# Optimization experiments

Hardware: AMD Instinct MI355X
Metric: run time of the kernel (lower is better)

Reference implementation:

```python
import jax, jax.numpy as jnp
import numpy as np

B, D, M, P, I, O = 256, 10, 32, 36, 8, 16
NUM_ITERATIONS = 3
EPS = 1e-07


def squash(s, axis=-1):
    sq = jnp.sum(s * s, axis=axis, keepdims=True)
    safe_norm = jnp.sqrt(sq + EPS)
    scale = sq / (1.0 + sq)
    return scale * (s / safe_norm)


def setup_inputs() -> dict:
    key = jax.random.key(0)
    kx, kw = jax.random.split(key)
    x = jax.random.normal(kx, (B, M, P, I), dtype=jnp.float32)
    # Parameter shape matches torch: [1, D, M, 1, O, I]
    W = 0.01 * jax.random.normal(kw, (1, D, M, 1, O, I), dtype=jnp.float32)
    return {"x": x, "W": W}


def reference(x, W):
    Wd = W[0, :, :, 0]  # [D, M, O, I]
    # u_hat: [B, D, M, P, O]
    u_hat = jnp.einsum('dmoi,bmpi->bdmpo', Wd, x)
    tu = jax.lax.stop_gradient(u_hat)
    b = jnp.zeros(u_hat.shape[:4], dtype=u_hat.dtype)  # [B, D, M, P]
    for _ in range(NUM_ITERATIONS - 1):
        c = jax.nn.softmax(b, axis=1)                 # over digit caps
        s = jnp.einsum('bdmp,bdmpo->bdo', c, tu)
        v = squash(s)
        b = b + jnp.einsum('bdmpo,bdo->bdmp', tu, v)
    # Final softmax over dim=3 (primary-cap axis), faithful to source
    c = jax.nn.softmax(b, axis=3)
    s = jnp.einsum('bdmp,bdmpo->bdo', c, u_hat)
    return squash(s)
```

## Files before the change

kernel.cpp:

```cpp
#include <hip/hip_runtime.h>
#include <math.h>

#define BB 256
#define DD 10
#define MM 32
#define PP 36
#define PH2 18
#define II 8
#define OO 16
#define NT 640
#define XS 288
#define RS 37
#define SWZ(m, c) ((((c) ^ ((m) & 7))) << 2)

__device__ __forceinline__ float dot8(const float4 a0, const float4 a1,
                                      const float4 b0, const float4 b1) {
    return a0.x*b0.x + a0.y*b0.y + a0.z*b0.z + a0.w*b0.w
         + a1.x*b1.x + a1.y*b1.y + a1.z*b1.z + a1.w*b1.w;
}

__global__ void __launch_bounds__(NT, 3) caps_routing(
    const float* __restrict__ x,
    const float* __restrict__ W,
    float* __restrict__ out)
{
    const int bidx = blockIdx.x;
    const int tid  = threadIdx.x;
    const int wave = tid >> 6;
    const int lane = tid & 63;
    const float* __restrict__ xb = x + (size_t)bidx * (MM*PP*II);

    __shared__ __align__(16) float xs  [MM*XS];
    __shared__ __align__(16) float z   [DD*MM*II];
    __shared__ __align__(16) float y   [DD*MM*II];
    __shared__ __align__(16) float ybar[MM*II];
    __shared__ __align__(16) float rinv[MM*RS];
    __shared__ __align__(16) float v_l [DD*OO];

    {
        const float4* xg = (const float4*)xb;
        #pragma unroll
        for (int k = 0; k < 4; ++k) {
            const int t = tid + k*NT;
            if (t < MM*72) {
                const int m = t / 72, c = t - m*72;
                *(float4*)(xs + m*XS + SWZ(m, c)) = xg[t];
            }
        }
    }
    __syncthreads();

    if (tid < MM*II) {
        const int m = tid >> 3, i = tid & 7;
        const int hi = i >> 2, lo = i & 3;
        const float* xrow = xs + m*XS;
        float acc = 0.f;
        #pragma unroll 6
        for (int p = 0; p < PP; ++p) acc += xrow[SWZ(m, 2*p + hi) + lo];
        ybar[tid] = 0.1f * acc;
    }
    __syncthreads();

    {
        const int d = wave;
        const int o = lane & 15, qq = lane >> 4;
        float s1 = 0.f;
        #pragma unroll
        for (int j = 0; j < 8; ++j) {
            const int m = qq*8 + j;
            const float4* wp = (const float4*)(W + ((size_t)((d*MM + m)*OO + o)) * II);
            const float4* yp = (const float4*)(ybar + m*II);
            s1 += dot8(wp[0], wp[1], yp[0], yp[1]);
        }
        s1 += __shfl_xor(s1, 16, 64);
        s1 += __shfl_xor(s1, 32, 64);
        float sq = s1 * s1;
        sq += __shfl_xor(sq, 1, 64);
        sq += __shfl_xor(sq, 2, 64);
        sq += __shfl_xor(sq, 4, 64);
        sq += __shfl_xor(sq, 8, 64);
        const float v1 = (sq / (1.f + sq)) * (s1 / sqrtf(sq + 1e-7f));
        if (lane < OO) v_l[d*OO + lane] = v1;

        const float4 vv0 = *(const float4*)(v_l + d*OO);
        const float4 vv1 = *(const float4*)(v_l + d*OO + 4);
        const float4 vv2 = *(const float4*)(v_l + d*OO + 8);
        const float4 vv3 = *(const float4*)(v_l + d*OO + 12);
        const float vs[16] = {vv0.x,vv0.y,vv0.z,vv0.w, vv1.x,vv1.y,vv1.z,vv1.w,
                              vv2.x,vv2.y,vv2.z,vv2.w, vv3.x,vv3.y,vv3.z,vv3.w};
        const int mz = lane >> 1, ihz = lane & 1;
        const float* wz = W + ((size_t)(d*MM + mz)*OO) * II + ihz*4;
        float a0 = 0.f, a1 = 0.f, a2 = 0.f, a3 = 0.f;
        #pragma unroll
        for (int o2 = 0; o2 < OO; ++o2) {
            const float4 wv = *(const float4*)(wz + o2*II);
            a0 += wv.x * vs[o2]; a1 += wv.y * vs[o2];
            a2 += wv.z * vs[o2]; a3 += wv.w * vs[o2];
        }
        *(float4*)(z + (d*MM + mz)*II + ihz*4) = make_float4(a0, a1, a2, a3);
    }
    __syncthreads();

    #pragma unroll
    for (int k = 0; k < 2; ++k) {
        const int t = tid + k*NT;
        if (t < MM*PP) {
            const int m = t / PP, p = t - m*PP;
            const float4 x0 = *(const float4*)(xs + m*XS + SWZ(m, 2*p));
            const float4 x1 = *(const float4*)(xs + m*XS + SWZ(m, 2*p + 1));
            float se = 0.f;
            #pragma unroll
            for (int d2 = 0; d2 < DD; ++d2) {
                const float4* zp = (const float4*)(z + (d2*MM + m)*II);
                se += __expf(dot8(x0, x1, zp[0], zp[1]));
            }
            rinv[m*RS + p] = 1.0f / se;
        }
    }
    __syncthreads();

    {
        const int d = wave;
        const float* __restrict__ zd = z + d*(MM*II);
        float* __restrict__ yd = y + d*(MM*II);

        const int mF = lane & 31;
        const int ph = lane >> 5;
        const float* xrow = xs + mF*XS;
        const float4 zf0 = *(const float4*)(zd + mF*II);
        const float4 zf1 = *(const float4*)(zd + mF*II + 4);

        {
            const float* rr = rinv + mF*RS + ph*PH2;
            float a0=0.f,a1=0.f,a2=0.f,a3=0.f,a4=0.f,a5=0.f,a6=0.f,a7=0.f;
            #pragma unroll 6
            for (int q = 0; q < PH2; ++q) {
                const int p = ph*PH2 + q;
                const float4 x0 = *(const float4*)(xrow + SWZ(mF, 2*p));
                const float4 x1 = *(const float4*)(xrow + SWZ(mF, 2*p + 1));
                const float e = __expf(dot8(x0, x1, zf0, zf1)) * rr[q];
                a0 += e*x0.x; a1 += e*x0.y; a2 += e*x0.z; a3 += e*x0.w;
                a4 += e*x1.x; a5 += e*x1.y; a6 += e*x1.z; a7 += e*x1.w;
            }
            a0 += __shfl_xor(a0, 32, 64); a1 += __shfl_xor(a1, 32, 64);
            a2 += __shfl_xor(a2, 32, 64); a3 += __shfl_xor(a3, 32, 64);
            a4 += __shfl_xor(a4, 32, 64); a5 += __shfl_xor(a5, 32, 64);
            a6 += __shfl_xor(a6, 32, 64); a7 += __shfl_xor(a7, 32, 64);
            const float4 wv = ph ? make_float4(a4,a5,a6,a7) : make_float4(a0,a1,a2,a3);
            *(float4*)(yd + mF*II + ph*4) = wv;
        }

        const int o = lane & 15, qq = lane >> 4;
        float s2 = 0.f;
        #pragma unroll
        for (int j = 0; j < 8; ++j) {
            const int m = qq*8 + j;
            const float4* wp = (const float4*)(W + ((size_t)((d*MM + m)*OO + o)) * II);
            const float4* yp = (const float4*)(yd + m*II);
            s2 += dot8(wp[0], wp[1], yp[0], yp[1]);
        }
        s2 += __shfl_xor(s2, 16, 64);
        s2 += __shfl_xor(s2, 32, 64);
        float sq = s2 * s2;
        sq += __shfl_xor(sq, 1, 64);
        sq += __shfl_xor(sq, 2, 64);
        sq += __shfl_xor(sq, 4, 64);
        sq += __shfl_xor(sq, 8, 64);
        const float v2 = (sq / (1.f + sq)) * (s2 / sqrtf(sq + 1e-7f));
        if (lane < OO) v_l[d*OO + lane] = v2;
        const float4 vv0 = *(const float4*)(v_l + d*OO);
        const float4 vv1 = *(const float4*)(v_l + d*OO + 4);
        const float4 vv2 = *(const float4*)(v_l + d*OO + 8);
        const float4 vv3 = *(const float4*)(v_l + d*OO + 12);
        const float vs[16] = {vv0.x,vv0.y,vv0.z,vv0.w, vv1.x,vv1.y,vv1.z,vv1.w,
                              vv2.x,vv2.y,vv2.z,vv2.w, vv3.x,vv3.y,vv3.z,vv3.w};

        float4 zf20, zf21;
        {
            const float* wz = W + ((size_t)(d*MM + mF)*OO) * II;
            float b0=0.f,b1=0.f,b2=0.f,b3=0.f,b4=0.f,b5=0.f,b6=0.f,b7=0.f;
            #pragma unroll
            for (int j = 0; j < 8; ++j) {
                const int o2 = ph*8 + j;
                const float4 w0 = *(const float4*)(wz + o2*II);
                const float4 w1 = *(const float4*)(wz + o2*II + 4);
                const float sv = vs[o2];
                b0 += w0.x*sv; b1 += w0.y*sv; b2 += w0.z*sv; b3 += w0.w*sv;
                b4 += w1.x*sv; b5 += w1.y*sv; b6 += w1.z*sv; b7 += w1.w*sv;
            }
            b0 += __shfl_xor(b0, 32, 64); b1 += __shfl_xor(b1, 32, 64);
            b2 += __shfl_xor(b2, 32, 64); b3 += __shfl_xor(b3, 32, 64);
            b4 += __shfl_xor(b4, 32, 64); b5 += __shfl_xor(b5, 32, 64);
            b6 += __shfl_xor(b6, 32, 64); b7 += __shfl_xor(b7, 32, 64);
            zf20 = make_float4(zf0.x + b0, zf0.y + b1, zf0.z + b2, zf0.w + b3);
            zf21 = make_float4(zf1.x + b4, zf1.y + b5, zf1.z + b6, zf1.w + b7);
        }

        {
            float se = 0.f;
            float a0=0.f,a1=0.f,a2=0.f,a3=0.f,a4=0.f,a5=0.f,a6=0.f,a7=0.f;
            #pragma unroll 6
            for (int q = 0; q < PH2; ++q) {
                const int p = ph*PH2 + q;
                const float4 x0 = *(const float4*)(xrow + SWZ(mF, 2*p));
                const float4 x1 = *(const float4*)(xrow + SWZ(mF, 2*p + 1));
                const float e = __expf(dot8(x0, x1, zf20, zf21));
                se += e;
                a0 += e*x0.x; a1 += e*x0.y; a2 += e*x0.z; a3 += e*x0.w;
                a4 += e*x1.x; a5 += e*x1.y; a6 += e*x1.z; a7 += e*x1.w;
            }
            se += __shfl_xor(se, 32, 64);
            a0 += __shfl_xor(a0, 32, 64); a1 += __shfl_xor(a1, 32, 64);
            a2 += __shfl_xor(a2, 32, 64); a3 += __shfl_xor(a3, 32, 64);
            a4 += __shfl_xor(a4, 32, 64); a5 += __shfl_xor(a5, 32, 64);
            a6 += __shfl_xor(a6, 32, 64); a7 += __shfl_xor(a7, 32, 64);
            const float rs = 1.f / se;
            const float4 wv = ph ? make_float4(a4*rs,a5*rs,a6*rs,a7*rs)
                                 : make_float4(a0*rs,a1*rs,a2*rs,a3*rs);
            *(float4*)(yd + mF*II + ph*4) = wv;
        }

        float s3 = 0.f;
        #pragma unroll
        for (int j = 0; j < 8; ++j) {
            const int m = qq*8 + j;
            const float4* wp = (const float4*)(W + ((size_t)((d*MM + m)*OO + o)) * II);
            const float4* yp = (const float4*)(yd + m*II);
            s3 += dot8(wp[0], wp[1], yp[0], yp[1]);
        }
        s3 += __shfl_xor(s3, 16, 64);
        s3 += __shfl_xor(s3, 32, 64);
        float sq3 = s3 * s3;
        sq3 += __shfl_xor(sq3, 1, 64);
        sq3 += __shfl_xor(sq3, 2, 64);
        sq3 += __shfl_xor(sq3, 4, 64);
        sq3 += __shfl_xor(sq3, 8, 64);
        const float r = (sq3 / (1.f + sq3)) * (s3 / sqrtf(sq3 + 1e-7f));
        if (lane < OO)
            out[(size_t)bidx * (DD*OO) + d*OO + o] = r;
    }
}

extern "C" void kernel_launch(void* const* d_in, const int* in_sizes, int n_in,
                              void* d_out, int out_size, void* d_ws, size_t ws_size,
                              hipStream_t stream) {
    (void)in_sizes; (void)n_in; (void)out_size; (void)d_ws; (void)ws_size;
    const float* x = (const float*)d_in[0];
    const float* W = (const float*)d_in[1];
    float* out = (float*)d_out;
    caps_routing<<<dim3(BB), dim3(NT), 0, stream>>>(x, W, out);
}
```

Measured before the change: 79.24 us.

## Hoist W into registers, compute ybar from global, use exp2 with prescaled logits

Loads the per-thread W slice into 64 registers once at kernel start and reuses it for all three s-reductions instead of reloading it from global memory each time. The ybar mean is computed straight from global x alongside the shared-memory fill, which removes one block barrier. Logits are prescaled by log2(e) so the hardware exp2 instruction replaces __expf. The extra live registers may reduce occupancy, given the launch bound of 640 threads with 3 blocks per CU.

```diff
diff --git a/kernel.cpp b/kernel.cpp
--- a/kernel.cpp
+++ b/kernel.cpp
@@ -12,6 +12,8 @@
 #define XS 288
 #define RS 37
 #define SWZ(m, c) ((((c) ^ ((m) & 7))) << 2)
+#define LOG2E 1.44269504088896f
+#define EXP2(v) __builtin_amdgcn_exp2f(v)
 
 __device__ __forceinline__ float dot8(const float4 a0, const float4 a1,
                                       const float4 b0, const float4 b1) {
@@ -37,6 +39,16 @@
     __shared__ __align__(16) float rinv[MM*RS];
     __shared__ __align__(16) float v_l [DD*OO];
 
+    const int d  = wave;
+    const int o  = lane & 15, qq = lane >> 4;
+
+    float4 wr0[8], wr1[8];
+    #pragma unroll
+    for (int j = 0; j < 8; ++j) {
+        const float4* wp = (const float4*)(W + ((size_t)((d*MM + qq*8 + j)*OO + o)) * II);
+        wr0[j] = wp[0]; wr1[j] = wp[1];
+    }
+
     {
         const float4* xg = (const float4*)xb;
         #pragma unroll
@@ -47,30 +59,23 @@
                 *(float4*)(xs + m*XS + SWZ(m, c)) = xg[t];
             }
         }
+        if (tid < MM*II) {
+            const int m = tid >> 3, i = tid & 7;
+            const float* xr = xb + m*(PP*II) + i;
+            float acc = 0.f;
+            #pragma unroll 6
+            for (int p = 0; p < PP; ++p) acc += xr[p*II];
+            ybar[tid] = 0.1f * acc;
+        }
     }
     __syncthreads();
 
-    if (tid < MM*II) {
-        const int m = tid >> 3, i = tid & 7;
-        const int hi = i >> 2, lo = i & 3;
-        const float* xrow = xs + m*XS;
-        float acc = 0.f;
-        #pragma unroll 6
-        for (int p = 0; p < PP; ++p) acc += xrow[SWZ(m, 2*p + hi) + lo];
-        ybar[tid] = 0.1f * acc;
-    }
-    __syncthreads();
-
     {
-        const int d = wave;
-        const int o = lane & 15, qq = lane >> 4;
         float s1 = 0.f;
         #pragma unroll
         for (int j = 0; j < 8; ++j) {
-            const int m = qq*8 + j;
-            const float4* wp = (const float4*)(W + ((size_t)((d*MM + m)*OO + o)) * II);
-            const float4* yp = (const float4*)(ybar + m*II);
-            s1 += dot8(wp[0], wp[1], yp[0], yp[1]);
+            const float4* yp = (const float4*)(ybar + (qq*8 + j)*II);
+            s1 += dot8(wr0[j], wr1[j], yp[0], yp[1]);
         }
         s1 += __shfl_xor(s1, 16, 64);
         s1 += __shfl_xor(s1, 32, 64);
@@ -97,7 +102,8 @@
             a0 += wv.x * vs[o2]; a1 += wv.y * vs[o2];
             a2 += wv.z * vs[o2]; a3 += wv.w * vs[o2];
         }
-        *(float4*)(z + (d*MM + mz)*II + ihz*4) = make_float4(a0, a1, a2, a3);
+        *(float4*)(z + (d*MM + mz)*II + ihz*4) =
+            make_float4(a0*LOG2E, a1*LOG2E, a2*LOG2E, a3*LOG2E);
     }
     __syncthreads();
 
@@ -112,7 +118,7 @@
             #pragma unroll
             for (int d2 = 0; d2 < DD; ++d2) {
                 const float4* zp = (const float4*)(z + (d2*MM + m)*II);
-                se += __expf(dot8(x0, x1, zp[0], zp[1]));
+                se += EXP2(dot8(x0, x1, zp[0], zp[1]));
             }
             rinv[m*RS + p] = 1.0f / se;
         }
@@ -120,7 +126,6 @@
     __syncthreads();
 
     {
-        const int d = wave;
         const float* __restrict__ zd = z + d*(MM*II);
         float* __restrict__ yd = y + d*(MM*II);
 
@@ -138,7 +143,7 @@
                 const int p = ph*PH2 + q;
                 const float4 x0 = *(const float4*)(xrow + SWZ(mF, 2*p));
                 const float4 x1 = *(const float4*)(xrow + SWZ(mF, 2*p + 1));
-                const float e = __expf(dot8(x0, x1, zf0, zf1)) * rr[q];
+                const float e = EXP2(dot8(x0, x1, zf0, zf1)) * rr[q];
                 a0 += e*x0.x; a1 += e*x0.y; a2 += e*x0.z; a3 += e*x0.w;
                 a4 += e*x1.x; a5 += e*x1.y; a6 += e*x1.z; a7 += e*x1.w;
             }
@@ -150,14 +155,11 @@
             *(float4*)(yd + mF*II + ph*4) = wv;
         }
 
-        const int o = lane & 15, qq = lane >> 4;
         float s2 = 0.f;
         #pragma unroll
         for (int j = 0; j < 8; ++j) {
-            const int m = qq*8 + j;
-            const float4* wp = (const float4*)(W + ((size_t)((d*MM + m)*OO + o)) * II);
-            const float4* yp = (const float4*)(yd + m*II);
-            s2 += dot8(wp[0], wp[1], yp[0], yp[1]);
+            const float4* yp = (const float4*)(yd + (qq*8 + j)*II);
+            s2 += dot8(wr0[j], wr1[j], yp[0], yp[1]);
         }
         s2 += __shfl_xor(s2, 16, 64);
         s2 += __shfl_xor(s2, 32, 64);
@@ -192,8 +194,10 @@
             b2 += __shfl_xor(b2, 32, 64); b3 += __shfl_xor(b3, 32, 64);
             b4 += __shfl_xor(b4, 32, 64); b5 += __shfl_xor(b5, 32, 64);
             b6 += __shfl_xor(b6, 32, 64); b7 += __shfl_xor(b7, 32, 64);
-            zf20 = make_float4(zf0.x + b0, zf0.y + b1, zf0.z + b2, zf0.w + b3);
-            zf21 = make_float4(zf1.x + b4, zf1.y + b5, zf1.z + b6, zf1.w + b7);
+            zf20 = make_float4(zf0.x + b0*LOG2E, zf0.y + b1*LOG2E,
+                               zf0.z + b2*LOG2E, zf0.w + b3*LOG2E);
+            zf21 = make_float4(zf1.x + b4*LOG2E, zf1.y + b5*LOG2E,
+                               zf1.z + b6*LOG2E, zf1.w + b7*LOG2E);
         }
 
         {
@@ -204,7 +208,7 @@
                 const int p = ph*PH2 + q;
                 const float4 x0 = *(const float4*)(xrow + SWZ(mF, 2*p));
                 const float4 x1 = *(const float4*)(xrow + SWZ(mF, 2*p + 1));
-                const float e = __expf(dot8(x0, x1, zf20, zf21));
+                const float e = EXP2(dot8(x0, x1, zf20, zf21));
                 se += e;
                 a0 += e*x0.x; a1 += e*x0.y; a2 += e*x0.z; a3 += e*x0.w;
                 a4 += e*x1.x; a5 += e*x1.y; a6 += e*x1.z; a7 += e*x1.w;
@@ -223,10 +227,8 @@
         float s3 = 0.f;
         #pragma unroll
         for (int j = 0; j < 8; ++j) {
-            const int m = qq*8 + j;
-            const float4* wp = (const float4*)(W + ((size_t)((d*MM + m)*OO + o)) * II);
-            const float4* yp = (const float4*)(yd + m*II);
-            s3 += dot8(wp[0], wp[1], yp[0], yp[1]);
+            const float4* yp = (const float4*)(yd + (qq*8 + j)*II);
+            s3 += dot8(wr0[j], wr1[j], yp[0], yp[1]);
         }
         s3 += __shfl_xor(s3, 16, 64);
         s3 += __shfl_xor(s3, 32, 64);
```

New measurement: 77.40 us. -2.3%, faster.
